# Kernel optimization log

Measured on AMD Instinct MI355X. Metric: run time of the kernel, lower is better.

Reference implementation:

```python
import jax, jax.numpy as jnp
import numpy as np

BATCH = 4096
DIM = 128
TEMP = 0.5
EPS = 1e-12  # F.normalize eps


def setup_inputs() -> dict:
    key = jax.random.key(0)
    k1, k2 = jax.random.split(key)
    emb_i = jax.random.normal(k1, (BATCH, DIM), dtype=jnp.float32)
    emb_j = jax.random.normal(k2, (BATCH, DIM), dtype=jnp.float32)
    return {"emb_i": emb_i, "emb_j": emb_j}


def _l2_normalize(x):
    # matches torch.nn.functional.normalize(x, dim=1, eps=1e-12)
    n = jnp.maximum(jnp.linalg.norm(x, axis=1, keepdims=True), EPS)
    return x / n


def reference(emb_i, emb_j):
    B = BATCH
    z_i = _l2_normalize(emb_i)
    z_j = _l2_normalize(emb_j)
    reps = jnp.concatenate([z_i, z_j], axis=0)            # [2B, D]
    # cosine similarity of unit vectors == Gram matrix
    sim = reps @ reps.T                                   # [2B, 2B]
    sim_ij = jnp.diagonal(sim, offset=B)                  # [B]
    sim_ji = jnp.diagonal(sim, offset=-B)                 # [B]
    positives = jnp.concatenate([sim_ij, sim_ji], axis=0) # [2B]
    neg_mask = 1.0 - jnp.eye(2 * B, dtype=sim.dtype)
    denom = jnp.sum(neg_mask * jnp.exp(sim / TEMP), axis=1)  # [2B]
    # -log(exp(pos/T) / denom) == -pos/T + log(denom)
    loss_partial = -(positives / TEMP) + jnp.log(denom)
    loss = jnp.sum(loss_partial) / (2 * B * 5)
    return loss
```

## Files before the change

kernel.cpp:

```cpp
#include <hip/hip_runtime.h>
#include <hip/hip_bf16.h>

#define B_ROWS 4096
#define DIMN 128
#define N2 8192
#define SQRT_CEXP 1.6986436f

using f32x4 = __attribute__((ext_vector_type(4))) float;
using i32x4 = __attribute__((ext_vector_type(4))) int;
using i32x8 = __attribute__((ext_vector_type(8))) int;
typedef long i64;


__global__ __launch_bounds__(256) void normpos_k(const float* __restrict__ emb_i,
                                                 const float* __restrict__ emb_j,
                                                 i64* __restrict__ zt,
                                                 float* __restrict__ pospart,
                                                 float* __restrict__ out) {
    const int t = threadIdx.x;
    if (blockIdx.x == 0 && t == 0) out[0] = 0.f;
    const int lr = t >> 4;
    const int s  = t & 15;
    const int p  = blockIdx.x * 16 + lr;
    const float4* ai = (const float4*)(emb_i + (size_t)p * DIMN + s * 8);
    const float4* bj = (const float4*)(emb_j + (size_t)p * DIMN + s * 8);
    float4 a0 = ai[0], a1 = ai[1];
    float4 b0 = bj[0], b1 = bj[1];
    float sa = a0.x*a0.x + a0.y*a0.y + a0.z*a0.z + a0.w*a0.w
             + a1.x*a1.x + a1.y*a1.y + a1.z*a1.z + a1.w*a1.w;
    float sb = b0.x*b0.x + b0.y*b0.y + b0.z*b0.z + b0.w*b0.w
             + b1.x*b1.x + b1.y*b1.y + b1.z*b1.z + b1.w*b1.w;
    float dp = a0.x*b0.x + a0.y*b0.y + a0.z*b0.z + a0.w*b0.w
             + a1.x*b1.x + a1.y*b1.y + a1.z*b1.z + a1.w*b1.w;
    #pragma unroll
    for (int d = 1; d < 16; d <<= 1) {
        sa += __shfl_xor(sa, d);
        sb += __shfl_xor(sb, d);
        dp += __shfl_xor(dp, d);
    }
    float ia = __builtin_amdgcn_rsqf(fmaxf(sa, 1e-24f));
    float ib = __builtin_amdgcn_rsqf(fmaxf(sb, 1e-24f));
    float fa = ia * SQRT_CEXP, fb = ib * SQRT_CEXP;

    int wa0 = __builtin_amdgcn_cvt_pk_fp8_f32(a0.x * fa, a0.y * fa, 0, false);
    wa0     = __builtin_amdgcn_cvt_pk_fp8_f32(a0.z * fa, a0.w * fa, wa0, true);
    int wa1 = __builtin_amdgcn_cvt_pk_fp8_f32(a1.x * fa, a1.y * fa, 0, false);
    wa1     = __builtin_amdgcn_cvt_pk_fp8_f32(a1.z * fa, a1.w * fa, wa1, true);
    i64 qa = ((i64)(unsigned)wa1 << 32) | (unsigned)wa0;
    int wb0 = __builtin_amdgcn_cvt_pk_fp8_f32(b0.x * fb, b0.y * fb, 0, false);
    wb0     = __builtin_amdgcn_cvt_pk_fp8_f32(b0.z * fb, b0.w * fb, wb0, true);
    int wb1 = __builtin_amdgcn_cvt_pk_fp8_f32(b1.x * fb, b1.y * fb, 0, false);
    wb1     = __builtin_amdgcn_cvt_pk_fp8_f32(b1.z * fb, b1.w * fb, wb1, true);
    i64 qb = ((i64)(unsigned)wb1 << 32) | (unsigned)wb0;

    const int slot = ((s >> 2) * 16 + lr) * 4 + (s & 3);
    zt[(size_t)blockIdx.x * 256 + slot] = qa;
    zt[(size_t)(256 + blockIdx.x) * 256 + slot] = qb;

    __shared__ float red[16];
    if (s == 0) red[lr] = dp * ia * ib;
    __syncthreads();
    if (t == 0) {
        float x = 0.f;
        #pragma unroll
        for (int i = 0; i < 16; ++i) x += red[i];
        pospart[blockIdx.x] = x;
    }
}

template <bool MASK>
__device__ __forceinline__ void accum_step(const f32x4 (&acc)[2][2],
                                           float (&ps)[2][4],
                                           int rb, int colbase, int rq, int fr) {
    #pragma unroll
    for (int m = 0; m < 2; ++m)
        #pragma unroll
        for (int n = 0; n < 2; ++n)
            #pragma unroll
            for (int j = 0; j < 4; ++j) {
                float e = __builtin_amdgcn_exp2f(acc[m][n][j]);
                if (MASK) {
                    if (rb + m * 16 + rq + j == colbase + n * 16 + fr) e = 0.f;
                }
                ps[m][j] += e;
            }
}

__global__ __launch_bounds__(512) void gram_k(const char* __restrict__ zt,
                                              const float* __restrict__ pospart,
                                              float* __restrict__ out) {
    const int t = threadIdx.x;
    const int lane = t & 63;
    const int w = t >> 6;
    const int p = blockIdx.x;
    const int rb = p * 32;
    const int fr = lane & 15;
    const int rq = (lane >> 4) * 4;

    const char* pa = zt + (size_t)(p * 2) * 2048 + lane * 32;
    const char* pb = zt + (size_t)(w * 64) * 2048 + lane * 32;

    i32x4 Alo[2], Ahi[2];
    #pragma unroll
    for (int m = 0; m < 2; ++m) {
        asm volatile("global_load_dwordx4 %0, %1, off"
                     : "=v"(Alo[m]) : "v"(pa + (size_t)m * 2048));
        asm volatile("global_load_dwordx4 %0, %1, off offset:16"
                     : "=v"(Ahi[m]) : "v"(pa + (size_t)m * 2048));
    }
    i32x4 Blo[2][2], Bhi[2][2];
    #pragma unroll
    for (int n = 0; n < 2; ++n) {
        asm volatile("global_load_dwordx4 %0, %1, off"
                     : "=v"(Blo[0][n]) : "v"(pb + (size_t)n * 2048));
        asm volatile("global_load_dwordx4 %0, %1, off offset:16"
                     : "=v"(Bhi[0][n]) : "v"(pb + (size_t)n * 2048));
    }
    asm volatile("s_waitcnt vmcnt(4)" ::: "memory");
    __builtin_amdgcn_sched_barrier(0);
    i32x8 A8[2];
    #pragma unroll
    for (int m = 0; m < 2; ++m)
        A8[m] = __builtin_shufflevector(Alo[m], Ahi[m], 0, 1, 2, 3, 4, 5, 6, 7);

    float ps[2][4] = {};
    #pragma unroll
    for (int s = 0; s < 32; ++s) {
        if (s < 31) {
            const char* pn = pb + (size_t)(s + 1) * 4096;
            #pragma unroll
            for (int n = 0; n < 2; ++n) {
                asm volatile("global_load_dwordx4 %0, %1, off"
                             : "=v"(Blo[(s + 1) & 1][n]) : "v"(pn + (size_t)n * 2048));
                asm volatile("global_load_dwordx4 %0, %1, off offset:16"
                             : "=v"(Bhi[(s + 1) & 1][n]) : "v"(pn + (size_t)n * 2048));
            }
            asm volatile("s_waitcnt vmcnt(4)" ::: "memory");
        } else {
            asm volatile("s_waitcnt vmcnt(0)" ::: "memory");
        }
        __builtin_amdgcn_sched_barrier(0);

        f32x4 acc[2][2] = {};
        __builtin_amdgcn_s_setprio(1);
        #pragma unroll
        for (int n = 0; n < 2; ++n) {
            i32x8 B8 = __builtin_shufflevector(Blo[s & 1][n], Bhi[s & 1][n],
                                               0, 1, 2, 3, 4, 5, 6, 7);
            #pragma unroll
            for (int m = 0; m < 2; ++m)
                acc[m][n] = __builtin_amdgcn_mfma_scale_f32_16x16x128_f8f6f4(
                    A8[m], B8, acc[m][n], 0, 0,
                    0, 0x7f7f7f7f, 0, 0x7f7f7f7f);
        }
        __builtin_amdgcn_s_setprio(0);

        const int cb = w * 1024 + s * 32;
        if (cb == rb) accum_step<true >(acc, ps, rb, cb, rq, fr);
        else          accum_step<false>(acc, ps, rb, cb, rq, fr);
    }

    #pragma unroll
    for (int m = 0; m < 2; ++m)
        #pragma unroll
        for (int j = 0; j < 4; ++j) {
            float v = ps[m][j];
            #pragma unroll
            for (int d = 1; d < 16; d <<= 1) v += __shfl_xor(v, d);
            ps[m][j] = v;
        }
    __shared__ float red[8][32];
    if (fr == 0) {
        #pragma unroll
        for (int m = 0; m < 2; ++m)
            #pragma unroll
            for (int j = 0; j < 4; ++j)
                red[w][m * 16 + rq + j] = ps[m][j];
    }
    __syncthreads();
    if (t < 32) {
        float dsum = 0.f;
        #pragma unroll
        for (int ww = 0; ww < 8; ++ww) dsum += red[ww][t];
        float lg = __builtin_amdgcn_logf(dsum);
        #pragma unroll
        for (int d = 1; d < 32; d <<= 1) lg += __shfl_xor(lg, d);
        if (t == 0) {
            float contrib = lg * 0.6931471805599453f;
            if (p < 128)
                contrib -= 4.0f * (pospart[2 * p] + pospart[2 * p + 1]);
            atomicAdd(out, contrib * (1.0f / (2.0f * B_ROWS * 5.0f)));
        }
    }
}

extern "C" void kernel_launch(void* const* d_in, const int* in_sizes, int n_in,
                              void* d_out, int out_size, void* d_ws, size_t ws_size,
                              hipStream_t stream) {
    const float* emb_i = (const float*)d_in[0];
    const float* emb_j = (const float*)d_in[1];
    i64* zt        = (i64*)d_ws;
    float* pospart = (float*)((char*)d_ws + (size_t)N2 * DIMN);

    normpos_k<<<256, 256, 0, stream>>>(emb_i, emb_j, zt, pospart, (float*)d_out);
    gram_k<<<256, 512, 0, stream>>>((const char*)zt, pospart, (float*)d_out);
}
```

Measured before the change: 29.23 us.

## Split gram columns across four blocks per row tile and add finalize kernel

The Gram kernel now launches 1024 blocks of 256 threads. Each block covers a quarter of the columns for a 32-row tile, where before 256 blocks of 512 threads each covered all columns. Per-row partial denominators go to a workspace buffer, and a new single-block finalize kernel sums them, takes logs, subtracts the positives and writes the loss. This removes the global atomic and the zero-init dependency. The aim is more blocks to fill the CUs and a shorter serial loop per wave, at the cost of an extra kernel launch and more A-tile reloads.

After: 26.78 us. 8.4% less time.

```diff
diff --git a/kernel.cpp b/kernel.cpp
--- a/kernel.cpp
+++ b/kernel.cpp
@@ -15,10 +15,8 @@
 __global__ __launch_bounds__(256) void normpos_k(const float* __restrict__ emb_i,
                                                  const float* __restrict__ emb_j,
                                                  i64* __restrict__ zt,
-                                                 float* __restrict__ pospart,
-                                                 float* __restrict__ out) {
+                                                 float* __restrict__ pospart) {
     const int t = threadIdx.x;
-    if (blockIdx.x == 0 && t == 0) out[0] = 0.f;
     const int lr = t >> 4;
     const int s  = t & 15;
     const int p  = blockIdx.x * 16 + lr;
@@ -71,7 +69,7 @@
 template <bool MASK>
 __device__ __forceinline__ void accum_step(const f32x4 (&acc)[2][2],
                                            float (&ps)[2][4],
-                                           int rb, int colbase, int rq, int fr) {
+                                           int rb, int cb, int rq, int fr) {
     #pragma unroll
     for (int m = 0; m < 2; ++m)
         #pragma unroll
@@ -80,25 +78,25 @@
             for (int j = 0; j < 4; ++j) {
                 float e = __builtin_amdgcn_exp2f(acc[m][n][j]);
                 if (MASK) {
-                    if (rb + m * 16 + rq + j == colbase + n * 16 + fr) e = 0.f;
+                    if (rb + m * 16 + rq + j == cb + n * 16 + fr) e = 0.f;
                 }
                 ps[m][j] += e;
             }
 }
 
-__global__ __launch_bounds__(512) void gram_k(const char* __restrict__ zt,
-                                              const float* __restrict__ pospart,
-                                              float* __restrict__ out) {
+__global__ __launch_bounds__(256) void gram_k(const char* __restrict__ zt,
+                                              float* __restrict__ rowpart) {
     const int t = threadIdx.x;
     const int lane = t & 63;
     const int w = t >> 6;
-    const int p = blockIdx.x;
+    const int p = blockIdx.x >> 2;
+    const int e = blockIdx.x & 3;
     const int rb = p * 32;
     const int fr = lane & 15;
     const int rq = (lane >> 4) * 4;
 
     const char* pa = zt + (size_t)(p * 2) * 2048 + lane * 32;
-    const char* pb = zt + (size_t)(w * 64) * 2048 + lane * 32;
+    const char* pb = zt + (size_t)(e * 128 + w * 32) * 2048 + lane * 32;
 
     i32x4 Alo[2], Ahi[2];
     #pragma unroll
@@ -125,8 +123,8 @@
 
     float ps[2][4] = {};
     #pragma unroll
-    for (int s = 0; s < 32; ++s) {
-        if (s < 31) {
+    for (int s = 0; s < 16; ++s) {
+        if (s < 15) {
             const char* pn = pb + (size_t)(s + 1) * 4096;
             #pragma unroll
             for (int n = 0; n < 2; ++n) {
@@ -155,7 +153,7 @@
         }
         __builtin_amdgcn_s_setprio(0);
 
-        const int cb = w * 1024 + s * 32;
+        const int cb = e * 2048 + w * 512 + s * 32;
         if (cb == rb) accum_step<true >(acc, ps, rb, cb, rq, fr);
         else          accum_step<false>(acc, ps, rb, cb, rq, fr);
     }
@@ -169,7 +167,7 @@
             for (int d = 1; d < 16; d <<= 1) v += __shfl_xor(v, d);
             ps[m][j] = v;
         }
-    __shared__ float red[8][32];
+    __shared__ float red[4][32];
     if (fr == 0) {
         #pragma unroll
         for (int m = 0; m < 2; ++m)
@@ -178,19 +176,33 @@
                 red[w][m * 16 + rq + j] = ps[m][j];
     }
     __syncthreads();
-    if (t < 32) {
-        float dsum = 0.f;
-        #pragma unroll
-        for (int ww = 0; ww < 8; ++ww) dsum += red[ww][t];
-        float lg = __builtin_amdgcn_logf(dsum);
-        #pragma unroll
-        for (int d = 1; d < 32; d <<= 1) lg += __shfl_xor(lg, d);
-        if (t == 0) {
-            float contrib = lg * 0.6931471805599453f;
-            if (p < 128)
-                contrib -= 4.0f * (pospart[2 * p] + pospart[2 * p + 1]);
-            atomicAdd(out, contrib * (1.0f / (2.0f * B_ROWS * 5.0f)));
-        }
+    if (t < 32)
+        rowpart[e * N2 + rb + t] = red[0][t] + red[1][t] + red[2][t] + red[3][t];
+}
+
+__global__ void finalize_k(const float* __restrict__ rowpart,
+                           const float* __restrict__ pospart,
+                           float* __restrict__ out) {
+    const int t = threadIdx.x;
+    float acc = 0.f;
+    #pragma unroll
+    for (int i = 0; i < 8; ++i) {
+        int r = t + i * 1024;
+        float d = rowpart[r] + rowpart[N2 + r] + rowpart[2 * N2 + r] + rowpart[3 * N2 + r];
+        acc += __builtin_amdgcn_logf(d);
+    }
+    acc *= 0.6931471805599453f;
+    if (t < 256) acc -= 4.0f * pospart[t];
+    #pragma unroll
+    for (int m = 32; m; m >>= 1) acc += __shfl_xor(acc, m);
+    __shared__ float red[16];
+    if ((t & 63) == 0) red[t >> 6] = acc;
+    __syncthreads();
+    if (t == 0) {
+        float x = 0.f;
+        #pragma unroll
+        for (int i = 0; i < 16; ++i) x += red[i];
+        out[0] = x / (float)(2 * B_ROWS * 5);
     }
 }
 
@@ -200,8 +212,10 @@
     const float* emb_i = (const float*)d_in[0];
     const float* emb_j = (const float*)d_in[1];
     i64* zt        = (i64*)d_ws;
-    float* pospart = (float*)((char*)d_ws + (size_t)N2 * DIMN);
-
-    normpos_k<<<256, 256, 0, stream>>>(emb_i, emb_j, zt, pospart, (float*)d_out);
-    gram_k<<<256, 512, 0, stream>>>((const char*)zt, pospart, (float*)d_out);
-}
+    float* rowpart = (float*)((char*)d_ws + (size_t)N2 * DIMN);
+    float* pospart = rowpart + 4 * N2;
+
+    normpos_k<<<256, 256, 0, stream>>>(emb_i, emb_j, zt, pospart);
+    gram_k<<<1024, 256, 0, stream>>>((const char*)zt, rowpart);
+    finalize_k<<<1, 1024, 0, stream>>>(rowpart, pospart, (float*)d_out);
+}
```
